# Kernel optimization log

Measured on AMD Instinct MI355X. Metric: run time of the kernel, lower is better.

The kernel has to match this reference:

```python
import jax, jax.numpy as jnp
import numpy as np

BATCH, SEQ, DIM = 8, 2048, 512
NUM_Q, CODEBOOK = 8, 1024


def setup_inputs() -> dict:
    key = jax.random.key(0)
    k1, k2 = jax.random.split(key)
    x = jax.random.normal(k1, (BATCH, SEQ, DIM), dtype=jnp.float32)
    # one codebook per quantizer (uniform codebook size -> stacked [q, c, d])
    codebooks = jax.random.normal(k2, (NUM_Q, CODEBOOK, DIM), dtype=jnp.float32)
    return {"x": x, "codebooks": codebooks}


def reference(x, codebooks):
    """Residual VQ (Algorithm 1, SoundStream). Sequential nearest-neighbor
    quantization of the residual with straight-through estimator.
    project_in/project_out are Identity (codebook_dim == dim).
    Returns (quantized_out [b,n,d], indices [b,n,q], commit_losses [q]).
    """
    residual = x
    quantized_out = jnp.zeros_like(x)
    all_indices = []
    all_losses = []
    num_q = codebooks.shape[0]
    for q in range(num_q):  # small fixed loop over quantizer layers
        cb = codebooks[q]  # [c, d]
        # argmin of squared euclidean distance; ||r||^2 is constant over codes
        scores = -2.0 * jnp.einsum('bnd,cd->bnc', residual, cb) \
                 + jnp.sum(cb * cb, axis=-1)  # [b, n, c]
        idx = jnp.argmin(scores, axis=-1)  # [b, n]
        quant = cb[idx]  # gather codes: [b, n, d]
        # commitment loss (mse of detached quantize vs layer input)
        commit = jnp.mean((jax.lax.stop_gradient(quant) - residual) ** 2)
        # straight-through estimator
        quant_st = residual + jax.lax.stop_gradient(quant - residual)
        quantized_out = quantized_out + quant_st
        residual = residual - jax.lax.stop_gradient(quant)
        all_indices.append(idx)
        all_losses.append(commit)
    indices = jnp.stack(all_indices, axis=-1)  # [b, n, q]
    losses = jnp.stack(all_losses)  # [q]
    return quantized_out, indices, losses
```

## Files before the change

### kernel.cpp

```cpp
#include <hip/hip_runtime.h>
#include <cstdint>
#include <cstddef>


#define BATCH 8
#define SEQ   2048
#define DIM   512
#define NUMQ  8
#define CODES 1024
#define NPTS  (BATCH*SEQ)
#define MPTS  64
#define NWG   (NPTS/MPTS)
#define NTHR  512
#define NCHUNK 32
#define CHUNK_BYTES 32768

#define OUT_IDX   (BATCH*SEQ*DIM)
#define OUT_LOSS  (OUT_IDX + BATCH*SEQ*NUMQ)

#define WS_LOSS   0
#define WS_CNORM  1024
#define WS_CBH    40960

typedef _Float16 f16x8  __attribute__((ext_vector_type(8)));
typedef _Float16 f16x4  __attribute__((ext_vector_type(4)));
typedef float    f32x16 __attribute__((ext_vector_type(16)));

__global__ void k_zero(double* loss) {
  if (threadIdx.x < NUMQ) loss[threadIdx.x] = 0.0;
}

__global__ void k_cnorm(const float* __restrict__ cb, float* __restrict__ cnorm) {
  int r = blockIdx.x * blockDim.x + threadIdx.x;
  const float* row = cb + (size_t)r * DIM;
  float s = 0.f;
  for (int d = 0; d < DIM; d += 4) {
    float4 v = *(const float4*)(row + d);
    s += v.x * v.x + v.y * v.y + v.z * v.z + v.w * v.w;
  }
  cnorm[r] = s;
}

__global__ void k_prep(const float* __restrict__ cb, unsigned char* __restrict__ cbH) {
  unsigned tid = blockIdx.x * blockDim.x + threadIdx.x;
  unsigned h  = tid & 1;
  unsigned r  = tid >> 1;
  unsigned c  = r & (CODES - 1);
  unsigned t2 = r >> 10;
  unsigned g  = t2 & 1;
  unsigned t3 = t2 >> 1;
  unsigned ks = t3 & 31;
  unsigned q  = t3 >> 5;
  unsigned k  = ks * 16 + g * 8 + h * 4;
  float4 v = *(const float4*)(cb + ((size_t)((q << 10) | c)) * DIM + k);
  f16x4 o;
  o[0] = (_Float16)v.x; o[1] = (_Float16)v.y; o[2] = (_Float16)v.z; o[3] = (_Float16)v.w;
  *(f16x4*)(cbH + (size_t)tid * 8) = o;
}

__device__ __forceinline__ void stage(const unsigned char* __restrict__ cbq, int ks,
                                      unsigned char* buf, int tid) {
  const unsigned char* src = cbq + (size_t)ks * CHUNK_BYTES + tid * 16;
  unsigned char* dst = buf + (tid & ~63) * 16;
  #pragma unroll
  for (int i = 0; i < 4; ++i)
    __builtin_amdgcn_global_load_lds(
        (const __attribute__((address_space(1))) void*)(src + i * 8192),
        (__attribute__((address_space(3))) void*)(dst + i * 8192), 16, 0, 0);
}

__launch_bounds__(NTHR, 2)
__global__ void k_main(const float* __restrict__ x, const float* __restrict__ cb,
                       const unsigned char* __restrict__ cbH,
                       const float* __restrict__ cnorm,
                       double* __restrict__ lossAcc,
                       float* __restrict__ out)
{
  __shared__ __align__(16) unsigned char Af[MPTS * DIM * 2];
  __shared__ __align__(16) unsigned char Bb[2][CHUNK_BYTES];
  __shared__ float          s1w[MPTS][8];
  __shared__ unsigned short id1w[MPTS][8];
  __shared__ unsigned short cand[MPTS][8][4];
  __shared__ unsigned char  ccnt[MPTS][8];
  __shared__ float          gmA[MPTS];
  __shared__ int            win0A[MPTS];
  __shared__ unsigned short idxs[MPTS][NUMQ];
  __shared__ double         lred[8];

  const int tid = threadIdx.x;
  const int cl  = tid & 63;
  const int w   = tid >> 6;
  const int l31 = cl & 31;
  const int l5  = cl >> 5;
  const int wg  = blockIdx.x;

  const int rp = tid >> 3;
  const int rj = tid & 7;
  const size_t gp = (size_t)wg * MPTS + rp;
  float4 r4[16];
  {
    const float4* xr = (const float4*)(x + gp * DIM + rj * 64);
    #pragma unroll
    for (int i = 0; i < 16; ++i) r4[i] = xr[i];
  }

  const int bBase = l5 * 16384 + (w * 128 + l31) * 16;

  for (int q = 0; q < NUMQ; ++q) {
    #pragma unroll
    for (int i = 0; i < 8; ++i) {
      float4 a = r4[2 * i], b = r4[2 * i + 1];
      f16x8 v;
      v[0] = (_Float16)a.x; v[1] = (_Float16)a.y; v[2] = (_Float16)a.z; v[3] = (_Float16)a.w;
      v[4] = (_Float16)b.x; v[5] = (_Float16)b.y; v[6] = (_Float16)b.z; v[7] = (_Float16)b.w;
      int sl = ((i << 3) | rj) ^ (rp & 31);
      *(f16x8*)(Af + rp * 1024 + (sl << 4)) = v;
    }
    __syncthreads();

    const unsigned char* cbq = cbH + (size_t)q * NCHUNK * CHUNK_BYTES;
    stage(cbq, 0, Bb[0], tid);
    stage(cbq, 1, Bb[1], tid);

    f32x16 acc[2][4];
    #pragma unroll
    for (int mt = 0; mt < 2; ++mt)
      #pragma unroll
      for (int nt = 0; nt < 4; ++nt)
        #pragma unroll
        for (int e = 0; e < 16; ++e) acc[mt][nt][e] = 0.0f;

    #pragma unroll 1
    for (int ks = 0; ks < NCHUNK; ++ks) {
      if (ks < NCHUNK - 1) asm volatile("s_waitcnt vmcnt(4)" ::: "memory");
      else                 asm volatile("s_waitcnt vmcnt(0)" ::: "memory");
      __builtin_amdgcn_s_barrier();
      const unsigned char* bufp = Bb[ks & 1];
      const int s5 = (ks << 1) | l5;
      const int sf = ((((s5 & 7) << 3) | (s5 >> 3)) ^ l31) << 4;
      f16x8 a0 = *(const f16x8*)(Af + l31 * 1024 + sf);
      f16x8 a1 = *(const f16x8*)(Af + 32768 + l31 * 1024 + sf);
      f16x8 b0 = *(const f16x8*)(bufp + bBase);
      f16x8 b1 = *(const f16x8*)(bufp + bBase + 512);
      f16x8 b2 = *(const f16x8*)(bufp + bBase + 1024);
      f16x8 b3 = *(const f16x8*)(bufp + bBase + 1536);
      __builtin_amdgcn_s_setprio(1);
      acc[0][0] = __builtin_amdgcn_mfma_f32_32x32x16_f16(a0, b0, acc[0][0], 0, 0, 0);
      acc[0][1] = __builtin_amdgcn_mfma_f32_32x32x16_f16(a0, b1, acc[0][1], 0, 0, 0);
      acc[0][2] = __builtin_amdgcn_mfma_f32_32x32x16_f16(a0, b2, acc[0][2], 0, 0, 0);
      acc[0][3] = __builtin_amdgcn_mfma_f32_32x32x16_f16(a0, b3, acc[0][3], 0, 0, 0);
      acc[1][0] = __builtin_amdgcn_mfma_f32_32x32x16_f16(a1, b0, acc[1][0], 0, 0, 0);
      acc[1][1] = __builtin_amdgcn_mfma_f32_32x32x16_f16(a1, b1, acc[1][1], 0, 0, 0);
      acc[1][2] = __builtin_amdgcn_mfma_f32_32x32x16_f16(a1, b2, acc[1][2], 0, 0, 0);
      acc[1][3] = __builtin_amdgcn_mfma_f32_32x32x16_f16(a1, b3, acc[1][3], 0, 0, 0);
      __builtin_amdgcn_s_setprio(0);
      asm volatile("s_waitcnt lgkmcnt(0)" ::: "memory");
      __builtin_amdgcn_s_barrier();
      if (ks + 2 < NCHUNK) stage(cbq, ks + 2, (unsigned char*)Bb[ks & 1], tid);
    }

    {
      const float* cnq = cnorm + (q << 10) + (w << 7) + l31;
      const float cn0 = cnq[0], cn1 = cnq[32], cn2 = cnq[64], cn3 = cnq[96];
      #pragma unroll
      for (int mt = 0; mt < 2; ++mt) {
        acc[mt][0] = acc[mt][0] * -2.0f + cn0;
        acc[mt][1] = acc[mt][1] * -2.0f + cn1;
        acc[mt][2] = acc[mt][2] * -2.0f + cn2;
        acc[mt][3] = acc[mt][3] * -2.0f + cn3;
      }
    }

    #pragma unroll
    for (int mt = 0; mt < 2; ++mt)
      #pragma unroll
      for (int r = 0; r < 16; ++r) {
        float s = acc[mt][0][r]; int bi = l31;
        if (acc[mt][1][r] < s) { s = acc[mt][1][r]; bi = 32 + l31; }
        if (acc[mt][2][r] < s) { s = acc[mt][2][r]; bi = 64 + l31; }
        if (acc[mt][3][r] < s) { s = acc[mt][3][r]; bi = 96 + l31; }
        #pragma unroll
        for (int m = 1; m < 32; m <<= 1) {
          float os = __shfl_xor(s, m); int ob = __shfl_xor(bi, m);
          if (os < s || (os == s && ob < bi)) { s = os; bi = ob; }
        }
        if (l31 == 0) {
          int p = mt * 32 + (r & 3) + 8 * (r >> 2) + 4 * l5;
          s1w[p][w] = s; id1w[p][w] = (unsigned short)bi;
        }
      }
    __syncthreads();

    if (tid < MPTS) {
      int p = tid;
      float bs = s1w[p][0]; int bi = id1w[p][0];
      #pragma unroll
      for (int ww = 1; ww < 8; ++ww) {
        float s = s1w[p][ww];
        if (s < bs) { bs = s; bi = ww * 128 + id1w[p][ww]; }
      }
      gmA[p] = bs; win0A[p] = bi;
    }
    __syncthreads();

    #pragma unroll
    for (int mt = 0; mt < 2; ++mt)
      #pragma unroll
      for (int r = 0; r < 16; ++r) {
        const int p0 = mt * 32 + (r & 3) + 8 * (r >> 2);
        const float g0 = gmA[p0], g1 = gmA[p0 + 4];
        const float lim0 = g0 + 1.5f + 1e-4f * fabsf(g0);
        const float lim1 = g1 + 1.5f + 1e-4f * fabsf(g1);
        const float lim = l5 ? lim1 : lim0;
        unsigned long long b0 = __ballot(acc[mt][0][r] <= lim);
        unsigned long long b1 = __ballot(acc[mt][1][r] <= lim);
        unsigned long long b2 = __ballot(acc[mt][2][r] <= lim);
        unsigned long long b3 = __ballot(acc[mt][3][r] <= lim);
        if (cl == 0 || cl == 32) {
          const int p = p0 + (cl >> 3);
          unsigned short* cd = &cand[p][w][0];
          unsigned m0 = (cl == 0) ? (unsigned)b0 : (unsigned)(b0 >> 32);
          unsigned m1 = (cl == 0) ? (unsigned)b1 : (unsigned)(b1 >> 32);
          unsigned m2 = (cl == 0) ? (unsigned)b2 : (unsigned)(b2 >> 32);
          unsigned m3 = (cl == 0) ? (unsigned)b3 : (unsigned)(b3 >> 32);
          int n = 0;
          while (m0 && n < 4) { int bt = __builtin_ctz(m0); m0 &= m0 - 1; cd[n++] = (unsigned short)(bt); }
          while (m1 && n < 4) { int bt = __builtin_ctz(m1); m1 &= m1 - 1; cd[n++] = (unsigned short)(32 + bt); }
          while (m2 && n < 4) { int bt = __builtin_ctz(m2); m2 &= m2 - 1; cd[n++] = (unsigned short)(64 + bt); }
          while (m3 && n < 4) { int bt = __builtin_ctz(m3); m3 &= m3 - 1; cd[n++] = (unsigned short)(96 + bt); }
          ccnt[p][w] = (unsigned char)n;
        }
      }
    __syncthreads();

    #pragma unroll 1
    for (int pp = 0; pp < 8; ++pp) {
      const int p = w * 8 + pp;
      int tot = 0;
      #pragma unroll
      for (int ww = 0; ww < 8; ++ww) tot += ccnt[p][ww];
      int winner;
      if (tot <= 1) {
        winner = win0A[p];
      } else {
        const size_t gpp = (size_t)wg * MPTS + p;
        double bs = 1.0e300, bs2 = 1.0e300; int bi = 0x7FFFFFFF;
        #pragma unroll 1
        for (int ww = 0; ww < 8; ++ww) {
          const int nn = ccnt[p][ww];
          #pragma unroll 1
          for (int si = 0; si < nn; ++si) {
            const int cc = ww * 128 + cand[p][ww][si];
            const float4* cr = (const float4*)(cb + ((size_t)q * CODES + cc) * DIM + (cl & 7) * 64);
            double dt = 0.0, cs = 0.0;
            #pragma unroll
            for (int i = 0; i < 16; ++i) {
              float4 cv = cr[i];
              dt += (double)r4[i].x * cv.x + (double)r4[i].y * cv.y
                  + (double)r4[i].z * cv.z + (double)r4[i].w * cv.w;
              cs += (double)cv.x * cv.x + (double)cv.y * cv.y
                  + (double)cv.z * cv.z + (double)cv.w * cv.w;
            }
            #pragma unroll
            for (int m = 1; m < 8; m <<= 1) { dt += __shfl_xor(dt, m); cs += __shfl_xor(cs, m); }
            double dtb = __shfl(dt, pp * 8), csb = __shfl(cs, pp * 8);
            double s = -2.0 * dtb + csb;
            if (s < bs) { bs2 = bs; bs = s; bi = cc; }
            else if (s < bs2) { bs2 = s; }
          }
        }
        if (bs2 - bs <= 1e-3 + 1e-6 * fabs(bs)) {
          bs = 1.0e300; bi = 0x7FFFFFFF;
          const float4* xr2 = (const float4*)(x + gpp * DIM + (cl & 7) * 64);
          #pragma unroll 1
          for (int ww = 0; ww < 8; ++ww) {
            const int nn = ccnt[p][ww];
            #pragma unroll 1
            for (int si = 0; si < nn; ++si) {
              const int cc = ww * 128 + cand[p][ww][si];
              const float4* cr = (const float4*)(cb + ((size_t)q * CODES + cc) * DIM + (cl & 7) * 64);
              double dt = 0.0, cs = 0.0;
              #pragma unroll 1
              for (int i = 0; i < 16; ++i) {
                float4 xv = xr2[i];
                double rhx = xv.x, rhy = xv.y, rhz = xv.z, rhw = xv.w;
                #pragma unroll 1
                for (int t2 = 0; t2 < q; ++t2) {
                  const float4* qr = (const float4*)(cb + ((size_t)t2 * CODES + idxs[p][t2]) * DIM + (cl & 7) * 64);
                  float4 qv = qr[i];
                  rhx -= (double)qv.x; rhy -= (double)qv.y;
                  rhz -= (double)qv.z; rhw -= (double)qv.w;
                }
                float4 cv = cr[i];
                dt += rhx * cv.x + rhy * cv.y + rhz * cv.z + rhw * cv.w;
                cs += (double)cv.x * cv.x + (double)cv.y * cv.y
                    + (double)cv.z * cv.z + (double)cv.w * cv.w;
              }
              #pragma unroll
              for (int m = 1; m < 8; m <<= 1) { dt += __shfl_xor(dt, m); cs += __shfl_xor(cs, m); }
              double dtb = __shfl(dt, pp * 8), csb = __shfl(cs, pp * 8);
              double s = -2.0 * dtb + csb;
              if (s < bs || (s == bs && cc < bi)) { bs = s; bi = cc; }
            }
          }
        }
        winner = bi;
      }
      if (cl == 0) idxs[p][q] = (unsigned short)winner;
    }

    {
      const int win = idxs[rp][q];
      const float4* cr = (const float4*)(cb + ((size_t)q * CODES + win) * DIM + rj * 64);
      double ls = 0.0;
      #pragma unroll
      for (int i = 0; i < 16; ++i) {
        float4 cv = cr[i];
        float dx = cv.x - r4[i].x, dy = cv.y - r4[i].y;
        float dz = cv.z - r4[i].z, dw = cv.w - r4[i].w;
        ls += (double)dx * dx + (double)dy * dy + (double)dz * dz + (double)dw * dw;
        r4[i].x -= cv.x; r4[i].y -= cv.y; r4[i].z -= cv.z; r4[i].w -= cv.w;
      }
      #pragma unroll
      for (int m = 1; m < 64; m <<= 1) ls += __shfl_xor(ls, m);
      if (cl == 0) lred[w] = ls;
      __syncthreads();
      if (tid == 0) {
        double t = lred[0] + lred[1] + lred[2] + lred[3]
                 + lred[4] + lred[5] + lred[6] + lred[7];
        atomicAdd(lossAcc + q, t);
      }
    }
  }

  {
    const float4* xr = (const float4*)(x + gp * DIM + rj * 64);
    float4* orow = (float4*)(out + gp * DIM + rj * 64);
    #pragma unroll
    for (int i = 0; i < 16; ++i) {
      float4 xv = xr[i];
      float4 o;
      o.x = xv.x - r4[i].x; o.y = xv.y - r4[i].y;
      o.z = xv.z - r4[i].z; o.w = xv.w - r4[i].w;
      orow[i] = o;
    }
  }
  if (tid < MPTS) {
    float* ob = out + OUT_IDX + ((size_t)wg * MPTS + tid) * NUMQ;
    #pragma unroll
    for (int j = 0; j < NUMQ; ++j) ob[j] = (float)idxs[tid][j];
  }
}

__global__ void k_fin(const double* __restrict__ loss, float* __restrict__ out) {
  int t = threadIdx.x;
  if (t < NUMQ)
    out[OUT_LOSS + t] = (float)(loss[t] / (double)((size_t)BATCH * SEQ * DIM));
}

extern "C" void kernel_launch(void* const* d_in, const int* in_sizes, int n_in,
                              void* d_out, int out_size, void* d_ws, size_t ws_size,
                              hipStream_t stream) {
  (void)in_sizes; (void)n_in; (void)out_size; (void)ws_size;
  const float* x  = (const float*)d_in[0];
  const float* cb = (const float*)d_in[1];
  float* out = (float*)d_out;
  char* ws = (char*)d_ws;
  double* loss = (double*)(ws + WS_LOSS);
  float* cnorm = (float*)(ws + WS_CNORM);
  unsigned char* cbH = (unsigned char*)(ws + WS_CBH);

  k_zero<<<1, 64, 0, stream>>>(loss);
  k_cnorm<<<NUMQ * CODES / 256, 256, 0, stream>>>(cb, cnorm);
  k_prep<<<NUMQ * NCHUNK * CHUNK_BYTES / 8 / 256, 256, 0, stream>>>(cb, cbH);
  k_main<<<NWG, NTHR, 0, stream>>>(x, cb, cbH, cnorm, loss, out);
  k_fin<<<1, 64, 0, stream>>>(loss, out);
}
```

Before: 642.2 us.

## Double workgroup to 16 waves and prefetch next quantizer codebook chunks across layers

Raises the block size from 512 to 1024 threads (16 waves), so each wave covers 64 codes instead of 128 and holds half the accumulator tiles and residual registers. The per-point rescoring and residual bookkeeping are remapped to 16 lanes per point. The staging of the first two codebook chunks for the next quantizer now starts during the last chunks of the current layer, so the per-layer pipeline start is hidden. This trades more barrier participants and per-wave overhead, plus an extra barrier per layer, for more waves and overlap per CU.

Result: slower. 728.5 us (+13.4%).

```diff
diff --git a/kernel.cpp b/kernel.cpp
--- a/kernel.cpp
+++ b/kernel.cpp
@@ -11,7 +11,8 @@
 #define NPTS  (BATCH*SEQ)
 #define MPTS  64
 #define NWG   (NPTS/MPTS)
-#define NTHR  512
+#define NTHR  1024
+#define NW    16
 #define NCHUNK 32
 #define CHUNK_BYTES 32768
 
@@ -63,13 +64,13 @@
   const unsigned char* src = cbq + (size_t)ks * CHUNK_BYTES + tid * 16;
   unsigned char* dst = buf + (tid & ~63) * 16;
   #pragma unroll
-  for (int i = 0; i < 4; ++i)
+  for (int i = 0; i < 2; ++i)
     __builtin_amdgcn_global_load_lds(
-        (const __attribute__((address_space(1))) void*)(src + i * 8192),
-        (__attribute__((address_space(3))) void*)(dst + i * 8192), 16, 0, 0);
-}
-
-__launch_bounds__(NTHR, 2)
+        (const __attribute__((address_space(1))) void*)(src + i * 16384),
+        (__attribute__((address_space(3))) void*)(dst + i * 16384), 16, 0, 0);
+}
+
+__launch_bounds__(NTHR, 4)
 __global__ void k_main(const float* __restrict__ x, const float* __restrict__ cb,
                        const unsigned char* __restrict__ cbH,
                        const float* __restrict__ cnorm,
@@ -78,14 +79,14 @@
 {
   __shared__ __align__(16) unsigned char Af[MPTS * DIM * 2];
   __shared__ __align__(16) unsigned char Bb[2][CHUNK_BYTES];
-  __shared__ float          s1w[MPTS][8];
-  __shared__ unsigned short id1w[MPTS][8];
-  __shared__ unsigned short cand[MPTS][8][4];
-  __shared__ unsigned char  ccnt[MPTS][8];
+  __shared__ float          s1w[MPTS][NW];
+  __shared__ unsigned short id1w[MPTS][NW];
+  __shared__ unsigned short cand[MPTS][NW][4];
+  __shared__ unsigned char  ccnt[MPTS][NW];
   __shared__ float          gmA[MPTS];
   __shared__ int            win0A[MPTS];
   __shared__ unsigned short idxs[MPTS][NUMQ];
-  __shared__ double         lred[8];
+  __shared__ double         lred[NW];
 
   const int tid = threadIdx.x;
   const int cl  = tid & 63;
@@ -94,46 +95,50 @@
   const int l5  = cl >> 5;
   const int wg  = blockIdx.x;
 
-  const int rp = tid >> 3;
-  const int rj = tid & 7;
+  const int rp = tid >> 4;
+  const int rj = tid & 15;
   const size_t gp = (size_t)wg * MPTS + rp;
-  float4 r4[16];
+  float4 r4[8];
   {
-    const float4* xr = (const float4*)(x + gp * DIM + rj * 64);
-    #pragma unroll
-    for (int i = 0; i < 16; ++i) r4[i] = xr[i];
-  }
-
-  const int bBase = l5 * 16384 + (w * 128 + l31) * 16;
+    const float4* xr = (const float4*)(x + gp * DIM + rj * 32);
+    #pragma unroll
+    for (int i = 0; i < 8; ++i) r4[i] = xr[i];
+  }
+
+  const int bBase = l5 * 16384 + (w * 64 + l31) * 16;
 
   for (int q = 0; q < NUMQ; ++q) {
-    #pragma unroll
-    for (int i = 0; i < 8; ++i) {
+    const unsigned char* cbq = cbH + (size_t)q * NCHUNK * CHUNK_BYTES;
+    if (q == 0) {
+      stage(cbq, 0, Bb[0], tid);
+      stage(cbq, 1, Bb[1], tid);
+    }
+    #pragma unroll
+    for (int i = 0; i < 4; ++i) {
       float4 a = r4[2 * i], b = r4[2 * i + 1];
       f16x8 v;
       v[0] = (_Float16)a.x; v[1] = (_Float16)a.y; v[2] = (_Float16)a.z; v[3] = (_Float16)a.w;
       v[4] = (_Float16)b.x; v[5] = (_Float16)b.y; v[6] = (_Float16)b.z; v[7] = (_Float16)b.w;
-      int sl = ((i << 3) | rj) ^ (rp & 31);
+      const int s = rj * 4 + i;
+      const int sl = (((s & 7) << 3) | (s >> 3)) ^ (rp & 31);
       *(f16x8*)(Af + rp * 1024 + (sl << 4)) = v;
     }
     __syncthreads();
 
-    const unsigned char* cbq = cbH + (size_t)q * NCHUNK * CHUNK_BYTES;
-    stage(cbq, 0, Bb[0], tid);
-    stage(cbq, 1, Bb[1], tid);
-
-    f32x16 acc[2][4];
+    f32x16 acc[2][2];
     #pragma unroll
     for (int mt = 0; mt < 2; ++mt)
       #pragma unroll
-      for (int nt = 0; nt < 4; ++nt)
+      for (int nt = 0; nt < 2; ++nt)
         #pragma unroll
         for (int e = 0; e < 16; ++e) acc[mt][nt][e] = 0.0f;
 
     #pragma unroll 1
     for (int ks = 0; ks < NCHUNK; ++ks) {
-      if (ks < NCHUNK - 1) asm volatile("s_waitcnt vmcnt(4)" ::: "memory");
-      else                 asm volatile("s_waitcnt vmcnt(0)" ::: "memory");
+      if (q == NUMQ - 1 && ks == NCHUNK - 1)
+        asm volatile("s_waitcnt vmcnt(0)" ::: "memory");
+      else
+        asm volatile("s_waitcnt vmcnt(2)" ::: "memory");
       __builtin_amdgcn_s_barrier();
       const unsigned char* bufp = Bb[ks & 1];
       const int s5 = (ks << 1) | l5;
@@ -142,32 +147,27 @@
       f16x8 a1 = *(const f16x8*)(Af + 32768 + l31 * 1024 + sf);
       f16x8 b0 = *(const f16x8*)(bufp + bBase);
       f16x8 b1 = *(const f16x8*)(bufp + bBase + 512);
-      f16x8 b2 = *(const f16x8*)(bufp + bBase + 1024);
-      f16x8 b3 = *(const f16x8*)(bufp + bBase + 1536);
       __builtin_amdgcn_s_setprio(1);
       acc[0][0] = __builtin_amdgcn_mfma_f32_32x32x16_f16(a0, b0, acc[0][0], 0, 0, 0);
       acc[0][1] = __builtin_amdgcn_mfma_f32_32x32x16_f16(a0, b1, acc[0][1], 0, 0, 0);
-      acc[0][2] = __builtin_amdgcn_mfma_f32_32x32x16_f16(a0, b2, acc[0][2], 0, 0, 0);
-      acc[0][3] = __builtin_amdgcn_mfma_f32_32x32x16_f16(a0, b3, acc[0][3], 0, 0, 0);
       acc[1][0] = __builtin_amdgcn_mfma_f32_32x32x16_f16(a1, b0, acc[1][0], 0, 0, 0);
       acc[1][1] = __builtin_amdgcn_mfma_f32_32x32x16_f16(a1, b1, acc[1][1], 0, 0, 0);
-      acc[1][2] = __builtin_amdgcn_mfma_f32_32x32x16_f16(a1, b2, acc[1][2], 0, 0, 0);
-      acc[1][3] = __builtin_amdgcn_mfma_f32_32x32x16_f16(a1, b3, acc[1][3], 0, 0, 0);
       __builtin_amdgcn_s_setprio(0);
       asm volatile("s_waitcnt lgkmcnt(0)" ::: "memory");
       __builtin_amdgcn_s_barrier();
-      if (ks + 2 < NCHUNK) stage(cbq, ks + 2, (unsigned char*)Bb[ks & 1], tid);
+      const int nid = ks + 2;
+      if (nid < NCHUNK) stage(cbq, nid, Bb[ks & 1], tid);
+      else if (q + 1 < NUMQ)
+        stage(cbq + (size_t)NCHUNK * CHUNK_BYTES, nid - NCHUNK, Bb[ks & 1], tid);
     }
 
     {
-      const float* cnq = cnorm + (q << 10) + (w << 7) + l31;
-      const float cn0 = cnq[0], cn1 = cnq[32], cn2 = cnq[64], cn3 = cnq[96];
+      const float* cnq = cnorm + (q << 10) + (w << 6) + l31;
+      const float cn0 = cnq[0], cn1 = cnq[32];
       #pragma unroll
       for (int mt = 0; mt < 2; ++mt) {
         acc[mt][0] = acc[mt][0] * -2.0f + cn0;
         acc[mt][1] = acc[mt][1] * -2.0f + cn1;
-        acc[mt][2] = acc[mt][2] * -2.0f + cn2;
-        acc[mt][3] = acc[mt][3] * -2.0f + cn3;
       }
     }
 
@@ -177,8 +177,6 @@
       for (int r = 0; r < 16; ++r) {
         float s = acc[mt][0][r]; int bi = l31;
         if (acc[mt][1][r] < s) { s = acc[mt][1][r]; bi = 32 + l31; }
-        if (acc[mt][2][r] < s) { s = acc[mt][2][r]; bi = 64 + l31; }
-        if (acc[mt][3][r] < s) { s = acc[mt][3][r]; bi = 96 + l31; }
         #pragma unroll
         for (int m = 1; m < 32; m <<= 1) {
           float os = __shfl_xor(s, m); int ob = __shfl_xor(bi, m);
@@ -195,9 +193,9 @@
       int p = tid;
       float bs = s1w[p][0]; int bi = id1w[p][0];
       #pragma unroll
-      for (int ww = 1; ww < 8; ++ww) {
+      for (int ww = 1; ww < NW; ++ww) {
         float s = s1w[p][ww];
-        if (s < bs) { bs = s; bi = ww * 128 + id1w[p][ww]; }
+        if (s < bs) { bs = s; bi = ww * 64 + id1w[p][ww]; }
       }
       gmA[p] = bs; win0A[p] = bi;
     }
@@ -214,31 +212,25 @@
         const float lim = l5 ? lim1 : lim0;
         unsigned long long b0 = __ballot(acc[mt][0][r] <= lim);
         unsigned long long b1 = __ballot(acc[mt][1][r] <= lim);
-        unsigned long long b2 = __ballot(acc[mt][2][r] <= lim);
-        unsigned long long b3 = __ballot(acc[mt][3][r] <= lim);
         if (cl == 0 || cl == 32) {
           const int p = p0 + (cl >> 3);
           unsigned short* cd = &cand[p][w][0];
           unsigned m0 = (cl == 0) ? (unsigned)b0 : (unsigned)(b0 >> 32);
           unsigned m1 = (cl == 0) ? (unsigned)b1 : (unsigned)(b1 >> 32);
-          unsigned m2 = (cl == 0) ? (unsigned)b2 : (unsigned)(b2 >> 32);
-          unsigned m3 = (cl == 0) ? (unsigned)b3 : (unsigned)(b3 >> 32);
           int n = 0;
-          while (m0 && n < 4) { int bt = __builtin_ctz(m0); m0 &= m0 - 1; cd[n++] = (unsigned short)(bt); }
+          while (m0 && n < 4) { int bt = __builtin_ctz(m0); m0 &= m0 - 1; cd[n++] = (unsigned short)bt; }
           while (m1 && n < 4) { int bt = __builtin_ctz(m1); m1 &= m1 - 1; cd[n++] = (unsigned short)(32 + bt); }
-          while (m2 && n < 4) { int bt = __builtin_ctz(m2); m2 &= m2 - 1; cd[n++] = (unsigned short)(64 + bt); }
-          while (m3 && n < 4) { int bt = __builtin_ctz(m3); m3 &= m3 - 1; cd[n++] = (unsigned short)(96 + bt); }
           ccnt[p][w] = (unsigned char)n;
         }
       }
     __syncthreads();
 
     #pragma unroll 1
-    for (int pp = 0; pp < 8; ++pp) {
-      const int p = w * 8 + pp;
+    for (int pp = 0; pp < 4; ++pp) {
+      const int p = w * 4 + pp;
       int tot = 0;
       #pragma unroll
-      for (int ww = 0; ww < 8; ++ww) tot += ccnt[p][ww];
+      for (int ww = 0; ww < NW; ++ww) tot += ccnt[p][ww];
       int winner;
       if (tot <= 1) {
         winner = win0A[p];
@@ -246,15 +238,15 @@
         const size_t gpp = (size_t)wg * MPTS + p;
         double bs = 1.0e300, bs2 = 1.0e300; int bi = 0x7FFFFFFF;
         #pragma unroll 1
-        for (int ww = 0; ww < 8; ++ww) {
+        for (int ww = 0; ww < NW; ++ww) {
           const int nn = ccnt[p][ww];
           #pragma unroll 1
           for (int si = 0; si < nn; ++si) {
-            const int cc = ww * 128 + cand[p][ww][si];
-            const float4* cr = (const float4*)(cb + ((size_t)q * CODES + cc) * DIM + (cl & 7) * 64);
+            const int cc = ww * 64 + cand[p][ww][si];
+            const float4* cr = (const float4*)(cb + ((size_t)q * CODES + cc) * DIM + (cl & 15) * 32);
             double dt = 0.0, cs = 0.0;
             #pragma unroll
-            for (int i = 0; i < 16; ++i) {
+            for (int i = 0; i < 8; ++i) {
               float4 cv = cr[i];
               dt += (double)r4[i].x * cv.x + (double)r4[i].y * cv.y
                   + (double)r4[i].z * cv.z + (double)r4[i].w * cv.w;
@@ -262,8 +254,8 @@
                   + (double)cv.z * cv.z + (double)cv.w * cv.w;
             }
             #pragma unroll
-            for (int m = 1; m < 8; m <<= 1) { dt += __shfl_xor(dt, m); cs += __shfl_xor(cs, m); }
-            double dtb = __shfl(dt, pp * 8), csb = __shfl(cs, pp * 8);
+            for (int m = 1; m < 16; m <<= 1) { dt += __shfl_xor(dt, m); cs += __shfl_xor(cs, m); }
+            double dtb = __shfl(dt, pp * 16), csb = __shfl(cs, pp * 16);
             double s = -2.0 * dtb + csb;
             if (s < bs) { bs2 = bs; bs = s; bi = cc; }
             else if (s < bs2) { bs2 = s; }
@@ -271,22 +263,22 @@
         }
         if (bs2 - bs <= 1e-3 + 1e-6 * fabs(bs)) {
           bs = 1.0e300; bi = 0x7FFFFFFF;
-          const float4* xr2 = (const float4*)(x + gpp * DIM + (cl & 7) * 64);
+          const float4* xr2 = (const float4*)(x + gpp * DIM + (cl & 15) * 32);
           #pragma unroll 1
-          for (int ww = 0; ww < 8; ++ww) {
+          for (int ww = 0; ww < NW; ++ww) {
             const int nn = ccnt[p][ww];
             #pragma unroll 1
             for (int si = 0; si < nn; ++si) {
-              const int cc = ww * 128 + cand[p][ww][si];
-              const float4* cr = (const float4*)(cb + ((size_t)q * CODES + cc) * DIM + (cl & 7) * 64);
+              const int cc = ww * 64 + cand[p][ww][si];
+              const float4* cr = (const float4*)(cb + ((size_t)q * CODES + cc) * DIM + (cl & 15) * 32);
               double dt = 0.0, cs = 0.0;
               #pragma unroll 1
-              for (int i = 0; i < 16; ++i) {
+              for (int i = 0; i < 8; ++i) {
                 float4 xv = xr2[i];
                 double rhx = xv.x, rhy = xv.y, rhz = xv.z, rhw = xv.w;
                 #pragma unroll 1
                 for (int t2 = 0; t2 < q; ++t2) {
-                  const float4* qr = (const float4*)(cb + ((size_t)t2 * CODES + idxs[p][t2]) * DIM + (cl & 7) * 64);
+                  const float4* qr = (const float4*)(cb + ((size_t)t2 * CODES + idxs[p][t2]) * DIM + (cl & 15) * 32);
                   float4 qv = qr[i];
                   rhx -= (double)qv.x; rhy -= (double)qv.y;
                   rhz -= (double)qv.z; rhw -= (double)qv.w;
@@ -297,8 +289,8 @@
                     + (double)cv.z * cv.z + (double)cv.w * cv.w;
               }
               #pragma unroll
-              for (int m = 1; m < 8; m <<= 1) { dt += __shfl_xor(dt, m); cs += __shfl_xor(cs, m); }
-              double dtb = __shfl(dt, pp * 8), csb = __shfl(cs, pp * 8);
+              for (int m = 1; m < 16; m <<= 1) { dt += __shfl_xor(dt, m); cs += __shfl_xor(cs, m); }
+              double dtb = __shfl(dt, pp * 16), csb = __shfl(cs, pp * 16);
               double s = -2.0 * dtb + csb;
               if (s < bs || (s == bs && cc < bi)) { bs = s; bi = cc; }
             }
@@ -311,10 +303,10 @@
 
     {
       const int win = idxs[rp][q];
-      const float4* cr = (const float4*)(cb + ((size_t)q * CODES + win) * DIM + rj * 64);
+      const float4* cr = (const float4*)(cb + ((size_t)q * CODES + win) * DIM + rj * 32);
       double ls = 0.0;
       #pragma unroll
-      for (int i = 0; i < 16; ++i) {
+      for (int i = 0; i < 8; ++i) {
         float4 cv = cr[i];
         float dx = cv.x - r4[i].x, dy = cv.y - r4[i].y;
         float dz = cv.z - r4[i].z, dw = cv.w - r4[i].w;
@@ -326,18 +318,20 @@
       if (cl == 0) lred[w] = ls;
       __syncthreads();
       if (tid == 0) {
-        double t = lred[0] + lred[1] + lred[2] + lred[3]
-                 + lred[4] + lred[5] + lred[6] + lred[7];
+        double t = 0.0;
+        #pragma unroll
+        for (int ww = 0; ww < NW; ++ww) t += lred[ww];
         atomicAdd(lossAcc + q, t);
       }
+      __syncthreads();
     }
   }
 
   {
-    const float4* xr = (const float4*)(x + gp * DIM + rj * 64);
-    float4* orow = (float4*)(out + gp * DIM + rj * 64);
-    #pragma unroll
-    for (int i = 0; i < 16; ++i) {
+    const float4* xr = (const float4*)(x + gp * DIM + rj * 32);
+    float4* orow = (float4*)(out + gp * DIM + rj * 32);
+    #pragma unroll
+    for (int i = 0; i < 8; ++i) {
       float4 xv = xr[i];
       float4 o;
       o.x = xv.x - r4[i].x; o.y = xv.y - r4[i].y;
```

## Give each wave private codebook staging slots and prefetch across quantizer layers

Applied to the files above, without the earlier changes.

Reorders the fp16 codebook layout so each wave's 128-code slice of a chunk is contiguous, then has every wave stage its own slice into a private double-buffered LDS slot. This removes the two block-wide barriers per K-chunk in the MFMA loop. Prefetching now continues across quantizer boundaries, so the first chunks of the next layer load during the argmin and refine phases. Two block barriers are added around the index and loss step to keep correctness.

Measured after the change: 632.1 us. Within noise of the previous version (-1.6%).

```diff
diff --git a/kernel.cpp b/kernel.cpp
--- a/kernel.cpp
+++ b/kernel.cpp
@@ -13,6 +13,7 @@
 #define NWG   (NPTS/MPTS)
 #define NTHR  512
 #define NCHUNK 32
+#define NCHUNK_TOT (NUMQ*NCHUNK)
 #define CHUNK_BYTES 32768
 
 #define OUT_IDX   (BATCH*SEQ*DIM)
@@ -42,31 +43,31 @@
 }
 
 __global__ void k_prep(const float* __restrict__ cb, unsigned char* __restrict__ cbH) {
-  unsigned tid = blockIdx.x * blockDim.x + threadIdx.x;
-  unsigned h  = tid & 1;
-  unsigned r  = tid >> 1;
-  unsigned c  = r & (CODES - 1);
-  unsigned t2 = r >> 10;
-  unsigned g  = t2 & 1;
-  unsigned t3 = t2 >> 1;
-  unsigned ks = t3 & 31;
-  unsigned q  = t3 >> 5;
-  unsigned k  = ks * 16 + g * 8 + h * 4;
-  float4 v = *(const float4*)(cb + ((size_t)((q << 10) | c)) * DIM + k);
+  unsigned u = blockIdx.x * blockDim.x + threadIdx.x;
+  unsigned h  = u & 1;
+  unsigned v  = u >> 1;
+  unsigned c  = v & 127;
+  unsigned g  = (v >> 7) & 1;
+  unsigned w  = (v >> 8) & 7;
+  unsigned ks = (v >> 11) & 31;
+  unsigned q  = v >> 16;
+  unsigned code = (w << 7) | c;
+  unsigned k = ks * 16 + g * 8 + h * 4;
+  float4 val = *(const float4*)(cb + ((size_t)((q << 10) | code)) * DIM + k);
   f16x4 o;
-  o[0] = (_Float16)v.x; o[1] = (_Float16)v.y; o[2] = (_Float16)v.z; o[3] = (_Float16)v.w;
-  *(f16x4*)(cbH + (size_t)tid * 8) = o;
-}
-
-__device__ __forceinline__ void stage(const unsigned char* __restrict__ cbq, int ks,
-                                      unsigned char* buf, int tid) {
-  const unsigned char* src = cbq + (size_t)ks * CHUNK_BYTES + tid * 16;
-  unsigned char* dst = buf + (tid & ~63) * 16;
+  o[0] = (_Float16)val.x; o[1] = (_Float16)val.y;
+  o[2] = (_Float16)val.z; o[3] = (_Float16)val.w;
+  *(f16x4*)(cbH + (size_t)u * 8) = o;
+}
+
+__device__ __forceinline__ void stage(const unsigned char* __restrict__ cbH, int n,
+                                      unsigned char* slot, int w, int cl) {
+  const unsigned char* src = cbH + (size_t)n * CHUNK_BYTES + (w << 12) + (cl << 4);
   #pragma unroll
   for (int i = 0; i < 4; ++i)
     __builtin_amdgcn_global_load_lds(
-        (const __attribute__((address_space(1))) void*)(src + i * 8192),
-        (__attribute__((address_space(3))) void*)(dst + i * 8192), 16, 0, 0);
+        (const __attribute__((address_space(1))) void*)(src + i * 1024),
+        (__attribute__((address_space(3))) void*)(slot + i * 1024), 16, 0, 0);
 }
 
 __launch_bounds__(NTHR, 2)
@@ -77,7 +78,7 @@
                        float* __restrict__ out)
 {
   __shared__ __align__(16) unsigned char Af[MPTS * DIM * 2];
-  __shared__ __align__(16) unsigned char Bb[2][CHUNK_BYTES];
+  __shared__ __align__(16) unsigned char Bs[8][2][4096];
   __shared__ float          s1w[MPTS][8];
   __shared__ unsigned short id1w[MPTS][8];
   __shared__ unsigned short cand[MPTS][8][4];
@@ -104,7 +105,11 @@
     for (int i = 0; i < 16; ++i) r4[i] = xr[i];
   }
 
-  const int bBase = l5 * 16384 + (w * 128 + l31) * 16;
+  unsigned char* mySlot = &Bs[w][0][0];
+  const int bOff = l5 * 2048 + l31 * 16;
+
+  stage(cbH, 0, mySlot, w, cl);
+  stage(cbH, 1, mySlot + 4096, w, cl);
 
   for (int q = 0; q < NUMQ; ++q) {
     #pragma unroll
@@ -118,10 +123,6 @@
     }
     __syncthreads();
 
-    const unsigned char* cbq = cbH + (size_t)q * NCHUNK * CHUNK_BYTES;
-    stage(cbq, 0, Bb[0], tid);
-    stage(cbq, 1, Bb[1], tid);
-
     f32x16 acc[2][4];
     #pragma unroll
     for (int mt = 0; mt < 2; ++mt)
@@ -132,18 +133,19 @@
 
     #pragma unroll 1
     for (int ks = 0; ks < NCHUNK; ++ks) {
-      if (ks < NCHUNK - 1) asm volatile("s_waitcnt vmcnt(4)" ::: "memory");
-      else                 asm volatile("s_waitcnt vmcnt(0)" ::: "memory");
-      __builtin_amdgcn_s_barrier();
-      const unsigned char* bufp = Bb[ks & 1];
+      if (q == NUMQ - 1 && ks == NCHUNK - 1)
+        asm volatile("s_waitcnt vmcnt(0)" ::: "memory");
+      else
+        asm volatile("s_waitcnt vmcnt(4)" ::: "memory");
+      const unsigned char* bufp = mySlot + ((ks & 1) << 12);
       const int s5 = (ks << 1) | l5;
       const int sf = ((((s5 & 7) << 3) | (s5 >> 3)) ^ l31) << 4;
       f16x8 a0 = *(const f16x8*)(Af + l31 * 1024 + sf);
       f16x8 a1 = *(const f16x8*)(Af + 32768 + l31 * 1024 + sf);
-      f16x8 b0 = *(const f16x8*)(bufp + bBase);
-      f16x8 b1 = *(const f16x8*)(bufp + bBase + 512);
-      f16x8 b2 = *(const f16x8*)(bufp + bBase + 1024);
-      f16x8 b3 = *(const f16x8*)(bufp + bBase + 1536);
+      f16x8 b0 = *(const f16x8*)(bufp + bOff);
+      f16x8 b1 = *(const f16x8*)(bufp + bOff + 512);
+      f16x8 b2 = *(const f16x8*)(bufp + bOff + 1024);
+      f16x8 b3 = *(const f16x8*)(bufp + bOff + 1536);
       __builtin_amdgcn_s_setprio(1);
       acc[0][0] = __builtin_amdgcn_mfma_f32_32x32x16_f16(a0, b0, acc[0][0], 0, 0, 0);
       acc[0][1] = __builtin_amdgcn_mfma_f32_32x32x16_f16(a0, b1, acc[0][1], 0, 0, 0);
@@ -155,8 +157,8 @@
       acc[1][3] = __builtin_amdgcn_mfma_f32_32x32x16_f16(a1, b3, acc[1][3], 0, 0, 0);
       __builtin_amdgcn_s_setprio(0);
       asm volatile("s_waitcnt lgkmcnt(0)" ::: "memory");
-      __builtin_amdgcn_s_barrier();
-      if (ks + 2 < NCHUNK) stage(cbq, ks + 2, (unsigned char*)Bb[ks & 1], tid);
+      const int n = (q << 5) + ks + 2;
+      if (n < NCHUNK_TOT) stage(cbH, n, mySlot + ((ks & 1) << 12), w, cl);
     }
 
     {
@@ -235,7 +237,7 @@
 
     #pragma unroll 1
     for (int pp = 0; pp < 8; ++pp) {
-      const int p = w * 8 + pp;
+      const int p = (w << 3) + pp;
       int tot = 0;
       #pragma unroll
       for (int ww = 0; ww < 8; ++ww) tot += ccnt[p][ww];
@@ -308,6 +310,7 @@
       }
       if (cl == 0) idxs[p][q] = (unsigned short)winner;
     }
+    __syncthreads();
 
     {
       const int win = idxs[rp][q];
@@ -330,6 +333,7 @@
                  + lred[4] + lred[5] + lred[6] + lred[7];
         atomicAdd(lossAcc + q, t);
       }
+      __syncthreads();
     }
   }
 
```
